# Performance work log

Hardware: AMD Instinct MI355X
Metric: run time of the kernel (lower is better)

## Reference

```python
import jax, jax.numpy as jnp
import numpy as np

B, S, DM, DC, L, NS = 4, 2048, 2048, 512, 4, 5  # batch, seq, d_model, d_cortical, n_layers, n_settle


def _ln(x, g, b):
    # torch nn.LayerNorm, eps=1e-5
    m = x.mean(-1, keepdims=True)
    v = ((x - m) ** 2).mean(-1, keepdims=True)
    return (x - m) * jax.lax.rsqrt(v + 1e-5) * g + b


def setup_inputs() -> dict:
    key = jax.random.key(0)
    ks = jax.random.split(key, 20)
    f = lambda k, sh: jax.random.normal(k, sh, jnp.float32) * 0.02
    return dict(
        qwen_final_hidden=jax.random.normal(ks[0], (B, S, DM), jnp.float32),
        obs=jax.random.normal(ks[1], (4, B, S, DM), jnp.float32),
        proj_W=f(ks[2], (4, DC, DM)), proj_b=f(ks[3], (4, DC)),
        fuse_W=f(ks[4], (DC, 4 * DC)), fuse_b=f(ks[5], (DC,)),
        up_W=f(ks[6], (L, DC, DC)), up_b=f(ks[7], (L, DC)),
        lateral_W=f(ks[8], (L, DC, DC)), lateral_b=f(ks[9], (L, DC)),
        precision_logit=f(ks[10], (L, DC)),
        ln_g=jnp.ones((L, DC), jnp.float32), ln_b=jnp.zeros((L, DC), jnp.float32),
        down_W=f(ks[11], (L - 1, DC, DC)), down_b=f(ks[12], (L - 1, DC)),
        out1_W=f(ks[13], (DC, DC)), out1_b=f(ks[14], (DC,)),
        out2_W=f(ks[15], (DM, DC)), out2_b=f(ks[16], (DM,)),
    )


def reference(qwen_final_hidden, obs, proj_W, proj_b, fuse_W, fuse_b,
              up_W, up_b, lateral_W, lateral_b, precision_logit,
              ln_g, ln_b, down_W, down_b, out1_W, out1_b, out2_W, out2_b):
    b, s, dm = qwen_final_hidden.shape
    # per-observed-layer input projections, concatenated along features
    proj = jnp.einsum('obsd,ocd->bsoc', obs, proj_W) + proj_b  # (B,S,4,DC)
    cat = proj.reshape(b, s, -1)
    fused = cat @ fuse_W.T + fuse_b                             # (B,S,DC)
    x0 = fused.reshape(b * s, DC)                               # per-token cortical input

    prec = jax.nn.sigmoid(precision_logit)                      # (L,DC)

    # initial bottom-up pass: activations = compress(x)
    acts = []
    x = x0
    for i in range(L):
        x = _ln(x @ up_W[i].T + up_b[i], ln_g[i], ln_b[i])
        acts.append(x)

    # settling iterations
    for _ in range(NS):
        # top-down predictions computed from pre-sweep activations
        preds = [None] * L
        for i in range(L - 1, 0, -1):
            if i < L - 1:  # top layer has no top-down weights
                preds[i - 1] = acts[i] @ down_W[i].T + down_b[i]
        x = x0
        for i in range(L):
            compressed = _ln(x @ up_W[i].T + up_b[i], ln_g[i], ln_b[i])
            target = preds[i] if preds[i] is not None else acts[i]
            werr = (compressed - target) * prec[i]
            lateral = acts[i] @ lateral_W[i].T + lateral_b[i]
            acts[i] = _ln(acts[i] + 0.5 * werr + 0.1 * lateral, ln_g[i], ln_b[i])
            x = acts[i]

    top = acts[-1]
    h = jax.nn.gelu(top @ out1_W.T + out1_b, approximate=False)
    correction = (h @ out2_W.T + out2_b).reshape(b, s, dm)
    return qwen_final_hidden + correction
```

## Files before the change

kernel.cpp:

```cpp
#include <hip/hip_runtime.h>
#include <hip/hip_bf16.h>
#include <math.h>

#define NTOK 8192
#define DMD  2048
#define DCC  512
#define TOKH 4194304

typedef __attribute__((ext_vector_type(8))) short short8;
typedef __attribute__((ext_vector_type(4))) float f32x4;

__device__ inline float bf2f(unsigned short u) {
    union { unsigned int i; float f; } x; x.i = ((unsigned int)u) << 16; return x.f;
}
__device__ inline unsigned short f2bf(float f) {
    union { float f; unsigned int i; } x; x.f = f;
    unsigned int u = x.i;
    return (unsigned short)((u + 0x7fffu + ((u >> 16) & 1u)) >> 16);
}

typedef const __attribute__((address_space(1))) unsigned int* gas1_t;
typedef __attribute__((address_space(3))) unsigned int* las3_t;
__device__ inline void async16(const void* g, void* l) {
    __builtin_amdgcn_global_load_lds(
        (gas1_t)g,
        (las3_t)(unsigned int)(unsigned long long)l, 16, 0, 0);
}

struct CvtArgs { const float* src[6]; };

__global__ __launch_bounds__(256)
void wcvt_kernel(CvtArgs ca, unsigned short* __restrict__ dst)
{
    const int total = 1310720;
    for (int i = blockIdx.x * 256 + threadIdx.x; i < total; i += gridDim.x * 256) {
        const float* sp; int base;
        if      (i <  262144) { sp = ca.src[0]; base = 0;       }
        else if (i <  524288) { sp = ca.src[1]; base = 262144;  }
        else if (i <  786432) { sp = ca.src[2]; base = 524288;  }
        else if (i <  983040) { sp = ca.src[3]; base = 786432;  }
        else if (i < 1048576) { sp = ca.src[4]; base = 983040;  }
        else                  { sp = ca.src[5]; base = 1048576; }
        float4 v = ((const float4*)sp)[i - base];
        ushort4 o;
        o.x = f2bf(v.x); o.y = f2bf(v.y); o.z = f2bf(v.z); o.w = f2bf(v.w);
        ((ushort4*)dst)[i] = o;
    }
}

__global__ __launch_bounds__(256)
void ptr_kernel(const float* __restrict__ src, unsigned short* __restrict__ dst)
{
    __shared__ float t[32][33];
    const int o  = blockIdx.z;
    const int jb = blockIdx.x * 32;
    const int kb = blockIdx.y * 32;
    const int r  = threadIdx.x >> 3;
    const int c4 = (threadIdx.x & 7) * 4;
    {
        const float* s = src + ((size_t)o * DCC + kb + r) * DMD + jb + c4;
        float4 v = *(const float4*)s;
        t[r][c4+0]=v.x; t[r][c4+1]=v.y; t[r][c4+2]=v.z; t[r][c4+3]=v.w;
    }
    __syncthreads();
    {
        ushort4 u;
        u.x = f2bf(t[c4+0][r]); u.y = f2bf(t[c4+1][r]);
        u.z = f2bf(t[c4+2][r]); u.w = f2bf(t[c4+3][r]);
        *(ushort4*)(dst + ((size_t)o * DMD + jb + r) * DCC + kb + c4) = u;
    }
}

__global__ __launch_bounds__(256)
void bprime_kernel(const float* __restrict__ fuse_W, const float* __restrict__ fuse_b,
                   const float* __restrict__ proj_b, float* __restrict__ bp)
{
    const int row = blockIdx.x * 8 + (threadIdx.x >> 5);
    const int l32 = threadIdx.x & 31;
    const float* r = fuse_W + (size_t)row * (4 * DCC) + l32 * 64;
    const float* p = proj_b + l32 * 64;
    float s = 0.f;
    #pragma unroll
    for (int k = 0; k < 64; k += 4) {
        float4 v = *(const float4*)(r + k);
        float4 q = *(const float4*)(p + k);
        s += v.x*q.x + v.y*q.y + v.z*q.z + v.w*q.w;
    }
    #pragma unroll
    for (int off = 16; off; off >>= 1) s += __shfl_xor(s, off, 64);
    if (l32 == 0) bp[row] = s + fuse_b[row];
}

struct GArgs {
    const unsigned short* A[6];
    const unsigned short* W[6];
    const float*          bias[6];
    const float*          add[6];
    void*                 C[6];
};

template<bool OUTF32, bool GELU>
__global__ __launch_bounds__(256)
void gemm16(GArgs ga, int lda, int ldw, int ldadd, int ldc, int K)
{
    __shared__ unsigned short As[128 * 32];
    __shared__ unsigned short Bs[128 * 32];

    const int z    = blockIdx.z;
    const int tid  = threadIdx.x;
    const int wave = tid >> 6;
    const int lane = tid & 63;

    const int nwg   = gridDim.x * gridDim.y;
    const int bid   = blockIdx.y * gridDim.x + blockIdx.x;
    const int swz   = (bid & 7) * (nwg >> 3) + (bid >> 3);
    const int bn    = (swz % gridDim.x) * 128;
    const int bm    = (swz / gridDim.x) * 128;

    const int wr   = wave >> 1;
    const int wc   = wave & 1;

    const unsigned short* Ap = ga.A[z];
    const unsigned short* Wp = ga.W[z];

    const int lrow = lane >> 2;
    const int lcol = (lane & 3) * 8;

    f32x4 acc[4][4] = {};

    for (int k0 = 0; k0 < K; k0 += 32) {
        #pragma unroll
        for (int r = 0; r < 2; ++r) {
            int c = wave + r * 4;
            async16(Ap + (size_t)(bm + c * 16 + lrow) * lda + k0 + lcol, As + c * 512);
            async16(Wp + (size_t)(bn + c * 16 + lrow) * ldw + k0 + lcol, Bs + c * 512);
        }
        __syncthreads();

        short8 af[4], bfr[4];
        #pragma unroll
        for (int i = 0; i < 4; ++i) {
            af[i]  = *(const short8*)&As[(wr * 64 + i * 16 + (lane & 15)) * 32 + (lane >> 4) * 8];
            bfr[i] = *(const short8*)&Bs[(wc * 64 + i * 16 + (lane & 15)) * 32 + (lane >> 4) * 8];
        }
        #pragma unroll
        for (int mi = 0; mi < 4; ++mi)
            #pragma unroll
            for (int ni = 0; ni < 4; ++ni)
                acc[mi][ni] = __builtin_amdgcn_mfma_f32_16x16x32_bf16(
                    af[mi], bfr[ni], acc[mi][ni], 0, 0, 0);
        __syncthreads();
    }

    const float* bias = ga.bias[z];
    const float* add  = ga.add[z];
    #pragma unroll
    for (int ni = 0; ni < 4; ++ni) {
        int col = bn + wc * 64 + ni * 16 + (lane & 15);
        float bv = bias ? bias[col] : 0.0f;
        #pragma unroll
        for (int mi = 0; mi < 4; ++mi) {
            #pragma unroll
            for (int r = 0; r < 4; ++r) {
                int row = bm + wr * 64 + mi * 16 + (lane >> 4) * 4 + r;
                float vv = acc[mi][ni][r] + bv;
                if (GELU) vv = 0.5f * vv * (1.0f + erff(vv * 0.7071067811865475f));
                if (OUTF32) {
                    if (add) vv += add[(size_t)row * ldadd + col];
                    ((float*)ga.C[z])[(size_t)row * ldc + col] = vv;
                } else {
                    ((unsigned short*)ga.C[z])[(size_t)row * ldc + col] = f2bf(vv);
                }
            }
        }
    }
}

__global__ __launch_bounds__(256)
void x0gemm(const float* __restrict__ obs,
            const unsigned short* __restrict__ M16,
            const float* __restrict__ bp,
            unsigned short* __restrict__ x0)
{
    __shared__ unsigned short As[2][128 * 32];
    __shared__ unsigned short Bs[2][128 * 32];

    const int tid  = threadIdx.x;
    const int wave = tid >> 6;
    const int lane = tid & 63;

    const int nwg = gridDim.x * gridDim.y;
    const int bid = blockIdx.y * gridDim.x + blockIdx.x;
    const int swz = (bid & 7) * (nwg >> 3) + (bid >> 3);
    const int bn  = (swz % gridDim.x) * 128;
    const int bm  = (swz / gridDim.x) * 128;

    const int wr = wave >> 1;
    const int wc = wave & 1;
    const int lrow = lane >> 2;
    const int lcol = (lane & 3) * 8;
    const int l15  = lane & 15;
    const int lh   = lane >> 4;

    const int srow = wave * 32 + (lane >> 2);
    const int scol = (lane & 3) * 8;

    f32x4 acc[4][4] = {};
    float4 pa[4];

    {
        const float* Ap = obs;
        pa[0] = *(const float4*)(Ap + (size_t)(bm + srow) * DMD + scol);
        pa[1] = *(const float4*)(Ap + (size_t)(bm + srow) * DMD + scol + 4);
        pa[2] = *(const float4*)(Ap + (size_t)(bm + srow + 16) * DMD + scol);
        pa[3] = *(const float4*)(Ap + (size_t)(bm + srow + 16) * DMD + scol + 4);
        #pragma unroll
        for (int r = 0; r < 2; ++r) {
            int c = wave + r * 4;
            async16(M16 + (size_t)(bn + c * 16 + lrow) * DMD + lcol, &Bs[0][c * 512]);
        }
        short8 o8;
        o8[0]=(short)f2bf(pa[0].x); o8[1]=(short)f2bf(pa[0].y);
        o8[2]=(short)f2bf(pa[0].z); o8[3]=(short)f2bf(pa[0].w);
        o8[4]=(short)f2bf(pa[1].x); o8[5]=(short)f2bf(pa[1].y);
        o8[6]=(short)f2bf(pa[1].z); o8[7]=(short)f2bf(pa[1].w);
        *(short8*)&As[0][srow * 32 + scol] = o8;
        o8[0]=(short)f2bf(pa[2].x); o8[1]=(short)f2bf(pa[2].y);
        o8[2]=(short)f2bf(pa[2].z); o8[3]=(short)f2bf(pa[2].w);
        o8[4]=(short)f2bf(pa[3].x); o8[5]=(short)f2bf(pa[3].y);
        o8[6]=(short)f2bf(pa[3].z); o8[7]=(short)f2bf(pa[3].w);
        *(short8*)&As[0][(srow + 16) * 32 + scol] = o8;
    }
    __syncthreads();

    for (int kk = 0; kk < 256; ++kk) {
        const int cur = kk & 1;
        if (kk < 255) {
            const int kk1 = kk + 1;
            const int o   = kk1 >> 6;
            const int k0  = (kk1 & 63) << 5;
            const float* Ap = obs + (size_t)o * NTOK * DMD;
            pa[0] = *(const float4*)(Ap + (size_t)(bm + srow) * DMD + k0 + scol);
            pa[1] = *(const float4*)(Ap + (size_t)(bm + srow) * DMD + k0 + scol + 4);
            pa[2] = *(const float4*)(Ap + (size_t)(bm + srow + 16) * DMD + k0 + scol);
            pa[3] = *(const float4*)(Ap + (size_t)(bm + srow + 16) * DMD + k0 + scol + 4);
            const unsigned short* Wp = M16 + (size_t)o * DCC * DMD;
            #pragma unroll
            for (int r = 0; r < 2; ++r) {
                int c = wave + r * 4;
                async16(Wp + (size_t)(bn + c * 16 + lrow) * DMD + k0 + lcol,
                        &Bs[cur ^ 1][c * 512]);
            }
        }
        short8 af[4], bfr[4];
        #pragma unroll
        for (int i = 0; i < 4; ++i) {
            af[i]  = *(const short8*)&As[cur][(wr * 64 + i * 16 + l15) * 32 + lh * 8];
            bfr[i] = *(const short8*)&Bs[cur][(wc * 64 + i * 16 + l15) * 32 + lh * 8];
        }
        #pragma unroll
        for (int mi = 0; mi < 4; ++mi)
            #pragma unroll
            for (int ni = 0; ni < 4; ++ni)
                acc[mi][ni] = __builtin_amdgcn_mfma_f32_16x16x32_bf16(
                    af[mi], bfr[ni], acc[mi][ni], 0, 0, 0);
        if (kk < 255) {
            short8 o8;
            o8[0]=(short)f2bf(pa[0].x); o8[1]=(short)f2bf(pa[0].y);
            o8[2]=(short)f2bf(pa[0].z); o8[3]=(short)f2bf(pa[0].w);
            o8[4]=(short)f2bf(pa[1].x); o8[5]=(short)f2bf(pa[1].y);
            o8[6]=(short)f2bf(pa[1].z); o8[7]=(short)f2bf(pa[1].w);
            *(short8*)&As[cur ^ 1][srow * 32 + scol] = o8;
            o8[0]=(short)f2bf(pa[2].x); o8[1]=(short)f2bf(pa[2].y);
            o8[2]=(short)f2bf(pa[2].z); o8[3]=(short)f2bf(pa[2].w);
            o8[4]=(short)f2bf(pa[3].x); o8[5]=(short)f2bf(pa[3].y);
            o8[6]=(short)f2bf(pa[3].z); o8[7]=(short)f2bf(pa[3].w);
            *(short8*)&As[cur ^ 1][(srow + 16) * 32 + scol] = o8;
        }
        __syncthreads();
    }

    #pragma unroll
    for (int ni = 0; ni < 4; ++ni) {
        int col = bn + wc * 64 + ni * 16 + l15;
        float bv = bp[col];
        #pragma unroll
        for (int mi = 0; mi < 4; ++mi)
            #pragma unroll
            for (int r = 0; r < 4; ++r) {
                int row = bm + wr * 64 + mi * 16 + lh * 4 + r;
                x0[(size_t)row * DCC + col] = f2bf(acc[mi][ni][r] + bv);
            }
    }
}

__device__ inline int csw(int rl, int col) {
    int s = ((rl >> 2) & 3) ^ (rl & 3);
    return rl * 512 + (col ^ (s << 4));
}

template<int MODE>
__global__ __launch_bounds__(512)
void gemm_fused(const unsigned short* __restrict__ Ap,
                const unsigned short* __restrict__ Wp,
                const float* __restrict__ bias,
                const float* __restrict__ g,
                const float* __restrict__ b,
                const unsigned short* a_in,
                const unsigned short* t_in,
                const unsigned short* __restrict__ lat_in,
                const float* __restrict__ logit,
                unsigned short* outp)
{
    __shared__ unsigned short Bs[2][512 * 32];
    __shared__ unsigned short As2[2][32 * 32];
    __shared__ float red[2][8][32];

    const int tid  = threadIdx.x;
    const int wave = tid >> 6;
    const int lane = tid & 63;
    const int lrow = lane >> 2;
    const int lc8  = (lane & 3) * 8;
    const int bm   = blockIdx.x * 32;
    const int l15  = lane & 15;
    const int lh   = lane >> 4;

    f32x4 acc[2][4] = {};

    if (wave < 2)
        async16(Ap + (size_t)(bm + wave * 16 + lrow) * DCC + lc8, &As2[0][wave * 512]);
    #pragma unroll
    for (int r = 0; r < 4; ++r)
        async16(Wp + (size_t)((r * 8 + wave) * 16 + lrow) * DCC + lc8,
                &Bs[0][(r * 8 + wave) * 512]);
    __syncthreads();

    for (int t = 0; t < 16; ++t) {
        const int cur = t & 1;
        if (t < 15) {
            const int k0 = (t + 1) * 32;
            if (wave < 2)
                async16(Ap + (size_t)(bm + wave * 16 + lrow) * DCC + k0 + lc8,
                        &As2[cur ^ 1][wave * 512]);
            #pragma unroll
            for (int r = 0; r < 4; ++r)
                async16(Wp + (size_t)((r * 8 + wave) * 16 + lrow) * DCC + k0 + lc8,
                        &Bs[cur ^ 1][(r * 8 + wave) * 512]);
        }
        short8 af[2], bfr[4];
        #pragma unroll
        for (int mi = 0; mi < 2; ++mi)
            af[mi] = *(const short8*)&As2[cur][(mi * 16 + l15) * 32 + lh * 8];
        #pragma unroll
        for (int ni = 0; ni < 4; ++ni)
            bfr[ni] = *(const short8*)&Bs[cur][(wave * 64 + ni * 16 + l15) * 32 + lh * 8];
        #pragma unroll
        for (int mi = 0; mi < 2; ++mi)
            #pragma unroll
            for (int ni = 0; ni < 4; ++ni)
                acc[mi][ni] = __builtin_amdgcn_mfma_f32_16x16x32_bf16(
                    af[mi], bfr[ni], acc[mi][ni], 0, 0, 0);
        __syncthreads();
    }

    float bv[4], gv[4], bbv[4];
    #pragma unroll
    for (int ni = 0; ni < 4; ++ni) {
        int col = wave * 64 + ni * 16 + l15;
        bv[ni] = bias[col]; gv[ni] = g[col]; bbv[ni] = b[col];
    }

    float ps[2][4], pq[2][4];
    #pragma unroll
    for (int mi = 0; mi < 2; ++mi)
        #pragma unroll
        for (int rr = 0; rr < 4; ++rr) {
            float s = 0.f, q = 0.f;
            #pragma unroll
            for (int ni = 0; ni < 4; ++ni) {
                float v = acc[mi][ni][rr] + bv[ni];
                acc[mi][ni][rr] = v;
                s += v; q += v * v;
            }
            #pragma unroll
            for (int off = 1; off < 16; off <<= 1) {
                s += __shfl_xor(s, off, 64);
                q += __shfl_xor(q, off, 64);
            }
            ps[mi][rr] = s; pq[mi][rr] = q;
        }
    if (l15 == 0) {
        #pragma unroll
        for (int mi = 0; mi < 2; ++mi)
            #pragma unroll
            for (int rr = 0; rr < 4; ++rr) {
                int rl = mi * 16 + lh * 4 + rr;
                red[0][wave][rl] = ps[mi][rr];
                red[1][wave][rl] = pq[mi][rr];
            }
    }
    __syncthreads();

    unsigned short* compS = &Bs[0][0];
    #pragma unroll
    for (int mi = 0; mi < 2; ++mi)
        #pragma unroll
        for (int rr = 0; rr < 4; ++rr) {
            int rl = mi * 16 + lh * 4 + rr;
            float s = 0.f, q = 0.f;
            #pragma unroll
            for (int w = 0; w < 8; ++w) { s += red[0][w][rl]; q += red[1][w][rl]; }
            float m1 = s * (1.0f / DCC);
            float r1 = rsqrtf(q * (1.0f / DCC) - m1 * m1 + 1e-5f);
            #pragma unroll
            for (int ni = 0; ni < 4; ++ni) {
                int col = wave * 64 + ni * 16 + l15;
                compS[csw(rl, col)] = f2bf((acc[mi][ni][rr] - m1) * r1 * gv[ni] + bbv[ni]);
            }
        }
    __syncthreads();

    const int c0 = lane * 8;
    if constexpr (MODE == 0) {
        #pragma unroll
        for (int rr = 0; rr < 4; ++rr) {
            const int rl = wave * 4 + rr;
            const size_t gbase = (size_t)(bm + rl) * DCC + c0;
            short8 cm = *(const short8*)&compS[csw(rl, c0)];
            *(short8*)(outp + gbase) = cm;
        }
    } else {
        float gr[8], br[8], pr[8];
        {
            float4 g0 = *(const float4*)(g + c0),     g1 = *(const float4*)(g + c0 + 4);
            float4 b0 = *(const float4*)(b + c0),     b1 = *(const float4*)(b + c0 + 4);
            float4 p0 = *(const float4*)(logit + c0), p1 = *(const float4*)(logit + c0 + 4);
            float gt[8] = {g0.x,g0.y,g0.z,g0.w,g1.x,g1.y,g1.z,g1.w};
            float bt[8] = {b0.x,b0.y,b0.z,b0.w,b1.x,b1.y,b1.z,b1.w};
            float pt[8] = {p0.x,p0.y,p0.z,p0.w,p1.x,p1.y,p1.z,p1.w};
            #pragma unroll
            for (int j = 0; j < 8; ++j) {
                gr[j] = gt[j]; br[j] = bt[j];
                pr[j] = 1.0f / (1.0f + __expf(-pt[j]));
            }
        }
        #pragma unroll
        for (int rr = 0; rr < 4; ++rr) {
            const int rl = wave * 4 + rr;
            const size_t gbase = (size_t)(bm + rl) * DCC + c0;
            short8 cm = *(const short8*)&compS[csw(rl, c0)];
            short8 ar = *(const short8*)(a_in + gbase);
            short8 tr = *(const short8*)(t_in + gbase);
            short8 lr = *(const short8*)(lat_in + gbase);
            float tv[8], s = 0.f, q = 0.f;
            #pragma unroll
            for (int j = 0; j < 8; ++j) {
                float val = bf2f((unsigned short)ar[j])
                          + 0.5f * (bf2f((unsigned short)cm[j]) - bf2f((unsigned short)tr[j])) * pr[j]
                          + 0.1f * bf2f((unsigned short)lr[j]);
                tv[j] = val; s += val; q += val * val;
            }
            #pragma unroll
            for (int off = 1; off < 64; off <<= 1) {
                s += __shfl_xor(s, off, 64);
                q += __shfl_xor(q, off, 64);
            }
            float m2 = s * (1.0f / DCC);
            float r2 = rsqrtf(q * (1.0f / DCC) - m2 * m2 + 1e-5f);
            short8 o;
            #pragma unroll
            for (int j = 0; j < 8; ++j)
                o[j] = (short)f2bf((tv[j] - m2) * r2 * gr[j] + br[j]);
            *(short8*)(outp + gbase) = o;
        }
    }
}

extern "C" void kernel_launch(void* const* d_in, const int* in_sizes, int n_in,
                              void* d_out, int out_size, void* d_ws, size_t ws_size,
                              hipStream_t stream)
{
    const float* qwen   = (const float*)d_in[0];
    const float* obs    = (const float*)d_in[1];
    const float* proj_W = (const float*)d_in[2];
    const float* proj_b = (const float*)d_in[3];
    const float* fuse_W = (const float*)d_in[4];
    const float* fuse_b = (const float*)d_in[5];
    const float* up_W   = (const float*)d_in[6];
    const float* up_b   = (const float*)d_in[7];
    const float* lat_W  = (const float*)d_in[8];
    const float* lat_b  = (const float*)d_in[9];
    const float* plogit = (const float*)d_in[10];
    const float* ln_g   = (const float*)d_in[11];
    const float* ln_b   = (const float*)d_in[12];
    const float* down_W = (const float*)d_in[13];
    const float* down_b = (const float*)d_in[14];
    const float* out1_W = (const float*)d_in[15];
    const float* out1_b = (const float*)d_in[16];
    const float* out2_W = (const float*)d_in[17];
    const float* out2_b = (const float*)d_in[18];
    float* out = (float*)d_out;

    unsigned short* wsu = (unsigned short*)d_ws;
    float*          bp     = (float*)wsu;
    unsigned short* h16    = wsu + 2048;
    unsigned short* x0b    = wsu + 16777216;
    unsigned short* acts16[4] = {
        wsu + 20971520, wsu + 20971520 + TOKH,
        wsu + 20971520 + 2 * TOKH, wsu + 20971520 + 3 * TOKH };
    unsigned short* w16    = wsu + 37748736;
    unsigned short* fuseW16 = w16;
    unsigned short* upW16   = w16 + 1048576;
    unsigned short* latW16  = w16 + 2097152;
    unsigned short* downW16 = w16 + 3145728;
    unsigned short* out1W16 = w16 + 3932160;
    unsigned short* out2W16 = w16 + 4194304;
    unsigned short* projT16 = wsu + 47185920;
    unsigned short* M16     = wsu + 51380224;

    unsigned short* outu = (unsigned short*)d_out;
    unsigned short* pred16a = outu;
    unsigned short* pred16b = outu + TOKH;
    unsigned short* lat16[4] = { outu + 2*TOKH, outu + 3*TOKH, outu + 4*TOKH, outu + 5*TOKH };

    dim3 blk(256);
    dim3 blk512(512);

    {
        CvtArgs ca;
        ca.src[0] = fuse_W; ca.src[1] = up_W;   ca.src[2] = lat_W;
        ca.src[3] = down_W; ca.src[4] = out1_W; ca.src[5] = out2_W;
        wcvt_kernel<<<dim3(2048), blk, 0, stream>>>(ca, w16);
    }
    ptr_kernel<<<dim3(DMD/32, DCC/32, 4), blk, 0, stream>>>(proj_W, projT16);
    bprime_kernel<<<dim3(DCC/8), blk, 0, stream>>>(fuse_W, fuse_b, proj_b, bp);

    {
        GArgs a{};
        for (int o = 0; o < 4; ++o) {
            a.A[o] = fuseW16 + o * DCC;
            a.W[o] = projT16 + (size_t)o * DMD * DCC;
            a.bias[o] = nullptr;
            a.C[o] = M16 + (size_t)o * DCC * DMD;
        }
        gemm16<false, false><<<dim3(DMD/128, DCC/128, 4), blk, 0, stream>>>(
            a, 4 * DCC, DCC, 0, DMD, DCC);
    }

    x0gemm<<<dim3(DCC/128, NTOK/128), blk, 0, stream>>>(obs, M16, bp, x0b);

    dim3 fgrid(NTOK / 32);

    for (int i = 0; i < 4; ++i) {
        gemm_fused<0><<<fgrid, blk512, 0, stream>>>(
            (i == 0) ? x0b : acts16[i - 1],
            upW16 + (size_t)i * DCC * DCC, up_b + i * DCC,
            ln_g + i * DCC, ln_b + i * DCC,
            nullptr, nullptr, nullptr, nullptr, acts16[i]);
    }

    for (int s = 0; s < 5; ++s) {
        {
            GArgs a{};
            a.A[0] = acts16[1]; a.W[0] = downW16 + (size_t)1 * DCC * DCC;
            a.bias[0] = down_b + 1 * DCC; a.C[0] = pred16a;
            a.A[1] = acts16[2]; a.W[1] = downW16 + (size_t)2 * DCC * DCC;
            a.bias[1] = down_b + 2 * DCC; a.C[1] = pred16b;
            for (int i = 0; i < 4; ++i) {
                a.A[2 + i] = acts16[i];
                a.W[2 + i] = latW16 + (size_t)i * DCC * DCC;
                a.bias[2 + i] = lat_b + i * DCC;
                a.C[2 + i] = lat16[i];
            }
            gemm16<false, false><<<dim3(DCC/128, NTOK/128, 6), blk, 0, stream>>>(
                a, DCC, DCC, 0, DCC, DCC);
        }
        for (int i = 0; i < 4; ++i) {
            const unsigned short* tgt =
                (i == 0) ? pred16a : (i == 1) ? pred16b : acts16[i];
            gemm_fused<1><<<fgrid, blk512, 0, stream>>>(
                (i == 0) ? x0b : acts16[i - 1],
                upW16 + (size_t)i * DCC * DCC, up_b + i * DCC,
                ln_g + i * DCC, ln_b + i * DCC,
                acts16[i], tgt, lat16[i], plogit + i * DCC, acts16[i]);
        }
    }

    {
        GArgs a{};
        a.A[0] = acts16[3]; a.W[0] = out1W16; a.bias[0] = out1_b; a.C[0] = h16;
        gemm16<false, true><<<dim3(DCC/128, NTOK/128, 1), blk, 0, stream>>>(
            a, DCC, DCC, 0, DCC, DCC);
    }
    {
        GArgs a{};
        a.A[0] = h16; a.W[0] = out2W16; a.bias[0] = out2_b;
        a.add[0] = qwen; a.C[0] = out;
        gemm16<true, false><<<dim3(DMD/128, NTOK/128, 1), blk, 0, stream>>>(
            a, DCC, DCC, DMD, DMD, DCC);
    }
}
```

Measured before the change: 1.590 ms.

## Split x0 GEMM K dimension across observed layers with separate reduction kernel

The x0 projection GEMM previously looped over all four observed layers' K range (256 steps) inside one 256-block grid. It now launches a 4x larger grid with one z-slice per observed layer, each writing fp32 partial sums, and a new kernel adds the four partials plus the bias and converts to bf16. This raises parallelism from 256 workgroups to 1024 on a large-CU GPU, at the cost of writing and re-reading 64 MB of fp32 partials and an extra launch.

```diff
diff --git a/kernel.cpp b/kernel.cpp
--- a/kernel.cpp
+++ b/kernel.cpp
@@ -179,8 +179,7 @@
 __global__ __launch_bounds__(256)
 void x0gemm(const float* __restrict__ obs,
             const unsigned short* __restrict__ M16,
-            const float* __restrict__ bp,
-            unsigned short* __restrict__ x0)
+            float* __restrict__ partial)
 {
     __shared__ unsigned short As[2][128 * 32];
     __shared__ unsigned short Bs[2][128 * 32];
@@ -188,12 +187,17 @@
     const int tid  = threadIdx.x;
     const int wave = tid >> 6;
     const int lane = tid & 63;
+    const int o    = blockIdx.z;
 
     const int nwg = gridDim.x * gridDim.y;
     const int bid = blockIdx.y * gridDim.x + blockIdx.x;
     const int swz = (bid & 7) * (nwg >> 3) + (bid >> 3);
     const int bn  = (swz % gridDim.x) * 128;
     const int bm  = (swz / gridDim.x) * 128;
+
+    const float* Ap          = obs + (size_t)o * NTOK * DMD;
+    const unsigned short* Wp = M16 + (size_t)o * DCC * DMD;
+    float* Cp                = partial + (size_t)o * NTOK * DCC;
 
     const int wr = wave >> 1;
     const int wc = wave & 1;
@@ -209,7 +213,6 @@
     float4 pa[4];
 
     {
-        const float* Ap = obs;
         pa[0] = *(const float4*)(Ap + (size_t)(bm + srow) * DMD + scol);
         pa[1] = *(const float4*)(Ap + (size_t)(bm + srow) * DMD + scol + 4);
         pa[2] = *(const float4*)(Ap + (size_t)(bm + srow + 16) * DMD + scol);
@@ -217,7 +220,7 @@
         #pragma unroll
         for (int r = 0; r < 2; ++r) {
             int c = wave + r * 4;
-            async16(M16 + (size_t)(bn + c * 16 + lrow) * DMD + lcol, &Bs[0][c * 512]);
+            async16(Wp + (size_t)(bn + c * 16 + lrow) * DMD + lcol, &Bs[0][c * 512]);
         }
         short8 o8;
         o8[0]=(short)f2bf(pa[0].x); o8[1]=(short)f2bf(pa[0].y);
@@ -233,18 +236,14 @@
     }
     __syncthreads();
 
-    for (int kk = 0; kk < 256; ++kk) {
+    for (int kk = 0; kk < 64; ++kk) {
         const int cur = kk & 1;
-        if (kk < 255) {
-            const int kk1 = kk + 1;
-            const int o   = kk1 >> 6;
-            const int k0  = (kk1 & 63) << 5;
-            const float* Ap = obs + (size_t)o * NTOK * DMD;
+        if (kk < 63) {
+            const int k0 = (kk + 1) << 5;
             pa[0] = *(const float4*)(Ap + (size_t)(bm + srow) * DMD + k0 + scol);
             pa[1] = *(const float4*)(Ap + (size_t)(bm + srow) * DMD + k0 + scol + 4);
             pa[2] = *(const float4*)(Ap + (size_t)(bm + srow + 16) * DMD + k0 + scol);
             pa[3] = *(const float4*)(Ap + (size_t)(bm + srow + 16) * DMD + k0 + scol + 4);
-            const unsigned short* Wp = M16 + (size_t)o * DCC * DMD;
             #pragma unroll
             for (int r = 0; r < 2; ++r) {
                 int c = wave + r * 4;
@@ -264,7 +263,7 @@
             for (int ni = 0; ni < 4; ++ni)
                 acc[mi][ni] = __builtin_amdgcn_mfma_f32_16x16x32_bf16(
                     af[mi], bfr[ni], acc[mi][ni], 0, 0, 0);
-        if (kk < 255) {
+        if (kk < 63) {
             short8 o8;
             o8[0]=(short)f2bf(pa[0].x); o8[1]=(short)f2bf(pa[0].y);
             o8[2]=(short)f2bf(pa[0].z); o8[3]=(short)f2bf(pa[0].w);
@@ -283,15 +282,33 @@
     #pragma unroll
     for (int ni = 0; ni < 4; ++ni) {
         int col = bn + wc * 64 + ni * 16 + l15;
-        float bv = bp[col];
         #pragma unroll
         for (int mi = 0; mi < 4; ++mi)
             #pragma unroll
             for (int r = 0; r < 4; ++r) {
                 int row = bm + wr * 64 + mi * 16 + lh * 4 + r;
-                x0[(size_t)row * DCC + col] = f2bf(acc[mi][ni][r] + bv);
-            }
-    }
+                Cp[(size_t)row * DCC + col] = acc[mi][ni][r];
+            }
+    }
+}
+
+__global__ __launch_bounds__(256)
+void x0red(const float* __restrict__ partial, const float* __restrict__ bp,
+           unsigned short* __restrict__ x0)
+{
+    const int i = blockIdx.x * 256 + threadIdx.x;
+    float4 a = ((const float4*)partial)[i];
+    float4 b = ((const float4*)(partial + TOKH))[i];
+    float4 c = ((const float4*)(partial + 2 * (size_t)TOKH))[i];
+    float4 d = ((const float4*)(partial + 3 * (size_t)TOKH))[i];
+    const int col = (i * 4) & (DCC - 1);
+    float4 bv = *(const float4*)(bp + col);
+    ushort4 o;
+    o.x = f2bf(a.x + b.x + c.x + d.x + bv.x);
+    o.y = f2bf(a.y + b.y + c.y + d.y + bv.y);
+    o.z = f2bf(a.z + b.z + c.z + d.z + bv.z);
+    o.w = f2bf(a.w + b.w + c.w + d.w + bv.w);
+    ((ushort4*)x0)[i] = o;
 }
 
 __device__ inline int csw(int rl, int col) {
@@ -517,6 +534,7 @@
     unsigned short* out2W16 = w16 + 4194304;
     unsigned short* projT16 = wsu + 47185920;
     unsigned short* M16     = wsu + 51380224;
+    float*          part32  = (float*)(wsu + 55574528);
 
     unsigned short* outu = (unsigned short*)d_out;
     unsigned short* pred16a = outu;
@@ -547,7 +565,8 @@
             a, 4 * DCC, DCC, 0, DMD, DCC);
     }
 
-    x0gemm<<<dim3(DCC/128, NTOK/128), blk, 0, stream>>>(obs, M16, bp, x0b);
+    x0gemm<<<dim3(DCC/128, NTOK/128, 4), blk, 0, stream>>>(obs, M16, part32);
+    x0red<<<dim3(TOKH/4/256), blk, 0, stream>>>(part32, bp, x0b);
 
     dim3 fgrid(NTOK / 32);
 
```

Result: faster. 1.551 ms (-2.5%).
